# Optimization experiments

Measured on AMD Instinct MI355X. Metric: run time of the kernel, lower is better.

Reference implementation:

```python
import jax, jax.numpy as jnp
import numpy as np

N = 100000  # nodes
K = 6       # kNN neighbors (includes self, loop=True)


def _knn_edges(pos_np, k):
    """Exact kNN with self-loops, chunked to bound memory. Returns (src, dst) int32."""
    n = pos_np.shape[0]
    idx = np.empty((n, k), dtype=np.int32)
    sq = (pos_np ** 2).sum(1)
    cs = 512
    for s in range(0, n, cs):
        e = min(s + cs, n)
        d = sq[s:e, None] - 2.0 * (pos_np[s:e] @ pos_np.T) + sq[None, :]
        idx[s:e] = np.argpartition(d, k, axis=1)[:, :k].astype(np.int32)
    src = idx.reshape(-1)                                  # neighbors j
    dst = np.repeat(np.arange(n, dtype=np.int32), k)       # centers i
    return src, dst


def _linear_init(key, fan_in, fan_out):
    k1, k2 = jax.random.split(key)
    s = 1.0 / np.sqrt(fan_in)
    W = jax.random.uniform(k1, (fan_in, fan_out), minval=-s, maxval=s, dtype=jnp.float32)
    b = jax.random.uniform(k2, (fan_out,), minval=-s, maxval=s, dtype=jnp.float32)
    return W, b


def setup_inputs() -> dict:
    rng = np.random.default_rng(0)
    pos_np = rng.standard_normal((N, 3)).astype(np.float32)
    src, dst = _knn_edges(pos_np, K)
    edge_index = jnp.asarray(np.stack([src, dst]))

    key = jax.random.key(0)
    ks = jax.random.split(key, 6)
    W1a, b1a = _linear_init(ks[0], 3 + 3, 32)
    W1b, b1b = _linear_init(ks[1], 32, 32)
    W2a, b2a = _linear_init(ks[2], 32 + 3, 64)
    W2b, b2b = _linear_init(ks[3], 64, 64)
    W3a, b3a = _linear_init(ks[4], 64 + 3, 128)
    W3b, b3b = _linear_init(ks[5], 128, 128)

    return dict(pos=jnp.asarray(pos_np), edge_index=edge_index,
                W1a=W1a, b1a=b1a, W1b=W1b, b1b=b1b,
                W2a=W2a, b2a=b2a, W2b=W2b, b2b=b2b,
                W3a=W3a, b3a=b3a, W3b=W3b, b3b=b3b)


def _pointnet_conv(x, pos, src, dst, Wa, ba, Wb, bb):
    # message per edge (j->i): local_nn(concat(x_j, pos_j - pos_i)); max-aggregate at i
    m = jnp.concatenate([x[src], pos[src] - pos[dst]], axis=-1)  # [E, Cin+3]
    m = jax.nn.relu(m @ Wa + ba) @ Wb + bb                       # [E, Cout]
    return jax.ops.segment_max(m, dst, num_segments=N)           # [N, Cout]


def reference(pos, edge_index, W1a, b1a, W1b, b1b, W2a, b2a, W2b, b2b, W3a, b3a, W3b, b3b):
    src, dst = edge_index[0], edge_index[1]
    h = jax.nn.relu(_pointnet_conv(pos, pos, src, dst, W1a, b1a, W1b, b1b))
    h = jax.nn.relu(_pointnet_conv(h, pos, src, dst, W2a, b2a, W2b, b2b))
    h = jax.nn.relu(_pointnet_conv(h, pos, src, dst, W3a, b3a, W3b, b3b))
    return h
```

## Files before the change

### kernel.cpp

```cpp
#include <hip/hip_runtime.h>

#define NODES 100000
#define KNN 6

typedef unsigned short u16t;
typedef __attribute__((ext_vector_type(8))) short bf16x8;
typedef __attribute__((ext_vector_type(4))) float f32x4;
union U16 { uint4 u; bf16x8 b; };

__device__ inline f32x4 mfma16(bf16x8 a, bf16x8 b, f32x4 c) {
    return __builtin_amdgcn_mfma_f32_16x16x32_bf16(a, b, c, 0, 0, 0);
}
__device__ inline unsigned top2(unsigned u1, unsigned u0) {
    return __builtin_amdgcn_perm(u1, u0, 0x07060302u);
}
__device__ inline u16t bf16_rn(float x) {
    unsigned u = __float_as_uint(x);
    return (u16t)((u + 0x7FFF + ((u >> 16) & 1)) >> 16);
}
__device__ inline float bf16_f(u16t h) {
    return __uint_as_float(((unsigned)h) << 16);
}
__device__ inline void split_store(u16t* hp, u16t* lp, float v) {
    const unsigned u = __float_as_uint(v);
    *hp = (u16t)(u >> 16);
    const float hif = __uint_as_float(u & 0xFFFF0000u);
    *lp = (u16t)(__float_as_uint(v - hif) >> 16);
}

template <int CIN_, int N_>
__device__ void prep_dev(const float* __restrict__ W,
                         uint4* __restrict__ fh, uint4* __restrict__ fl, int idx) {
    constexpr int KT = (CIN_ + 31) / 32;
    constexpr int NTt = N_ / 16;
    if (idx >= NTt * KT * 64) return;
    const int lane = idx & 63;
    const int fk = idx >> 6;
    const int kt = fk % KT, t = fk / KT;
    const int n = t * 16 + (lane & 15);
    const int kbase = kt * 32 + (lane >> 4) * 8;
    unsigned h[4], l[4];
    for (int p = 0; p < 4; p++) {
        u16t hh[2], ll[2];
        for (int q = 0; q < 2; q++) {
            const int c = kbase + 2 * p + q;
            const float w = (c < CIN_) ? W[(size_t)c * N_ + n] : 0.f;
            const u16t hi = bf16_rn(w);
            hh[q] = hi;
            ll[q] = bf16_rn(w - bf16_f(hi));
        }
        h[p] = (unsigned)hh[0] | ((unsigned)hh[1] << 16);
        l[p] = (unsigned)ll[0] | ((unsigned)ll[1] << 16);
    }
    fh[idx] = make_uint4(h[0], h[1], h[2], h[3]);
    fl[idx] = make_uint4(l[0], l[1], l[2], l[3]);
}

__global__ void prep_all(const float* W1a, const float* W1b,
                         const float* W2a, const float* W2b,
                         const float* W3a, const float* W3b, uint4* wf) {
    const int b = blockIdx.x, t = threadIdx.x;
    if (b == 0)      prep_dev<6, 32>(W1a, wf + 0, wf + 128, t);
    else if (b == 1) prep_dev<32, 32>(W1b, wf + 256, wf + 384, t);
    else if (b == 2) prep_dev<32, 64>(W2a, wf + 512, wf + 768, t);
    else if (b < 5)  prep_dev<64, 64>(W2b, wf + 1024, wf + 1536, (b - 3) * 256 + t);
    else if (b < 11) prep_dev<67, 128>(W3a, wf + 2048, wf + 3584, (b - 5) * 256 + t);
    else             prep_dev<128, 128>(W3b, wf + 5120, wf + 7168, (b - 11) * 256 + t);
}

template <int CX, int H, int NWAVE, int NB, bool OUTP, bool DPOS>
__global__ __launch_bounds__(NWAVE * 64, (NWAVE == 2 && H >= 64) ? 3 : 4)
void pnconv_mfma(
    const u16t* __restrict__ xh, const u16t* __restrict__ xl,
    const float* __restrict__ pos, const int* __restrict__ ei,
    const uint4* __restrict__ wfa_hi, const uint4* __restrict__ wfa_lo,
    const float* __restrict__ ba,
    const uint4* __restrict__ wfb_hi, const uint4* __restrict__ wfb_lo,
    const float* __restrict__ bb,
    const float* __restrict__ wpos,
    float* __restrict__ outf, u16t* __restrict__ oh, u16t* __restrict__ ol)
{
    constexpr int NTH = NWAVE * 64;
    constexpr int CIN = DPOS ? CX : CX + 3;
    constexpr int K1T = (CIN + 31) / 32;
    constexpr int K2T = H / 32;
    constexpr int NW = (H / 16) / NWAVE;
    constexpr int E = NB * KNN;
    constexpr int MT1 = E / 16;
    constexpr int MT2 = E / 16;
    constexpr int K1P = K1T * 32 + 8;
    constexpr int K2P = K2T * 32 + 8;
    constexpr int APL = E * K1P;
    constexpr int HPL = E * K2P;
    constexpr int SM = (2 * APL > 2 * HPL) ? 2 * APL : 2 * HPL;
    static_assert(E % 48 == 0 && E <= NTH, "tile shape");
    static_assert(MT2 % 3 == 0, "slot perm needs m-triples");
    static_assert(!DPOS || (2 * APL + E * 8) <= SM, "dpos overlay fits");

    __shared__ __align__(16) u16t smem[SM];
    __shared__ int srcs[E];
    float* const dpf = (float*)&smem[2 * APL];

    const int tid = threadIdx.x;
    const int lane = tid & 63, wv = tid >> 6;
    const int l15 = lane & 15, quad = lane >> 4;
    const int node0 = blockIdx.x * NB;
    const long e0 = (long)node0 * KNN;

    if (tid < E) srcs[tid] = ei[e0 + tid];

    U16 wah[2][NW], wal[2][NW];
#pragma unroll
    for (int t = 0; t < NW; t++) {
        const int fi = ((wv * NW + t) * K1T) * 64 + lane;
        wah[0][t].u = wfa_hi[fi];
        wal[0][t].u = wfa_lo[fi];
    }
    f32x4 wpp[NW][3];
    if constexpr (DPOS) {
#pragma unroll
        for (int t = 0; t < NW; t++)
#pragma unroll
            for (int d = 0; d < 3; d++)
                wpp[t][d] = *(const f32x4*)&wpos[(size_t)(CX + d) * H +
                                                (wv * NW + t) * 16 + quad * 4];
    }
    __syncthreads();

    if constexpr (CX % 8 == 0) {
        constexpr int C8 = CX / 8;
        for (int i = tid; i < E * C8; i += NTH) {
            const int e = i / C8, c0 = i % C8;
            const int c = (c0 + e) & (C8 - 1);
            const size_t sb = (size_t)srcs[e] * CX + c * 8;
            *(uint4*)&smem[e * K1P + c * 8] = *(const uint4*)&xh[sb];
            *(uint4*)&smem[APL + e * K1P + c * 8] = *(const uint4*)&xl[sb];
        }
    }
    for (int i = tid; i < E * 3; i += NTH) {
        const int e = i / 3, d = i - 3 * (i / 3);
        const int s = srcs[e], nd = node0 + e / KNN;
        const float sp = pos[3 * s + d];
        const float dl = sp - pos[3 * nd + d];
        if constexpr (DPOS) {
            dpf[e * 4 + d] = dl;
        } else {
            if constexpr (CX == 3)
                split_store(&smem[e * K1P + d], &smem[APL + e * K1P + d], sp);
            split_store(&smem[e * K1P + CX + d], &smem[APL + e * K1P + CX + d], dl);
        }
    }
    if constexpr (!DPOS) {
        constexpr int PADA = (CIN + 7) & ~7;
        constexpr int NU4 = (K1P - PADA) / 8;
        for (int i = tid; i < 2 * E; i += NTH) {
            const int pl = (i >= E) ? 1 : 0;
            const int e = i - pl * E;
            u16t* row = &smem[pl * APL + e * K1P];
            for (int k = CIN; k < PADA; k++) row[k] = 0;
            for (int j = 0; j < NU4; j++) *(uint4*)&row[PADA + j * 8] = make_uint4(0, 0, 0, 0);
        }
    }
    __syncthreads();

    f32x4 acc1[NW][MT1];
#pragma unroll
    for (int t = 0; t < NW; t++)
#pragma unroll
        for (int m = 0; m < MT1; m++) acc1[t][m] = (f32x4){0.f, 0.f, 0.f, 0.f};

#pragma unroll
    for (int kt = 0; kt < K1T; kt++) {
        const int cur = kt & 1, nxt = cur ^ 1;
        if (kt + 1 < K1T) {
#pragma unroll
            for (int t = 0; t < NW; t++) {
                const int fi = ((wv * NW + t) * K1T + kt + 1) * 64 + lane;
                wah[nxt][t].u = wfa_hi[fi];
                wal[nxt][t].u = wfa_lo[fi];
            }
        }
#pragma unroll
        for (int m = 0; m < MT1; m++) {
            const u16t* p = &smem[(m * 16 + l15) * K1P + kt * 32 + quad * 8];
            U16 dh, dl;
            dh.u = *(const uint4*)p;
            dl.u = *(const uint4*)(p + APL);
#pragma unroll
            for (int t = 0; t < NW; t++) {
                acc1[t][m] = mfma16(wah[cur][t].b, dh.b, acc1[t][m]);
                acc1[t][m] = mfma16(wah[cur][t].b, dl.b, acc1[t][m]);
                acc1[t][m] = mfma16(wal[cur][t].b, dh.b, acc1[t][m]);
            }
        }
    }

    U16 wbh[2][NW], wbl[2][NW];
#pragma unroll
    for (int t = 0; t < NW; t++) {
        const int fi = ((wv * NW + t) * K2T) * 64 + lane;
        wbh[0][t].u = wfb_hi[fi];
        wbl[0][t].u = wfb_lo[fi];
    }

    if constexpr (DPOS) {
#pragma unroll
        for (int m = 0; m < MT1; m++) {
            const f32x4 dp = *(const f32x4*)&dpf[(m * 16 + l15) * 4];
#pragma unroll
            for (int t = 0; t < NW; t++)
#pragma unroll
                for (int j = 0; j < 4; j++)
                    acc1[t][m][j] += wpp[t][0][j] * dp[0] + wpp[t][1][j] * dp[1]
                                   + wpp[t][2][j] * dp[2];
        }
    }
    __syncthreads();

#pragma unroll
    for (int t = 0; t < NW; t++) {
        const int khb = (wv * NW + t) * 16 + quad * 4;
        const float4 bs = *(const float4*)&ba[khb];
#pragma unroll
        for (int m = 0; m < MT1; m++) {
            const float v0 = fmaxf(acc1[t][m][0] + bs.x, 0.f);
            const float v1 = fmaxf(acc1[t][m][1] + bs.y, 0.f);
            const float v2 = fmaxf(acc1[t][m][2] + bs.z, 0.f);
            const float v3 = fmaxf(acc1[t][m][3] + bs.w, 0.f);
            const unsigned u0 = __float_as_uint(v0), u1 = __float_as_uint(v1);
            const unsigned u2 = __float_as_uint(v2), u3 = __float_as_uint(v3);
            uint2 hw, lw;
            hw.x = top2(u1, u0);
            hw.y = top2(u3, u2);
            const float l0 = v0 - __uint_as_float(u0 & 0xFFFF0000u);
            const float l1 = v1 - __uint_as_float(u1 & 0xFFFF0000u);
            const float l2 = v2 - __uint_as_float(u2 & 0xFFFF0000u);
            const float l3 = v3 - __uint_as_float(u3 & 0xFFFF0000u);
            lw.x = top2(__float_as_uint(l1), __float_as_uint(l0));
            lw.y = top2(__float_as_uint(l3), __float_as_uint(l2));
            u16t* wp = &smem[(m * 16 + l15) * K2P + khb];
            *(uint2*)wp = hw;
            *(uint2*)(wp + HPL) = lw;
        }
    }
    __syncthreads();

    int eaddr[MT2];
#pragma unroll
    for (int m = 0; m < MT2; m++) {
        const int nd_s = (m / 3) * 8 + 2 * (l15 >> 2) + ((l15 >> 1) & 1);
        const int i_s = (m % 3) * 2 + (l15 & 1);
        eaddr[m] = (nd_s * KNN + i_s) * K2P + quad * 8;
    }

    f32x4 acc2[NW][MT2];
#pragma unroll
    for (int t = 0; t < NW; t++)
#pragma unroll
        for (int m = 0; m < MT2; m++) acc2[t][m] = (f32x4){0.f, 0.f, 0.f, 0.f};

#pragma unroll
    for (int kt = 0; kt < K2T; kt++) {
        const int cur = kt & 1, nxt = cur ^ 1;
        if (kt + 1 < K2T) {
#pragma unroll
            for (int t = 0; t < NW; t++) {
                const int fi = ((wv * NW + t) * K2T + kt + 1) * 64 + lane;
                wbh[nxt][t].u = wfb_hi[fi];
                wbl[nxt][t].u = wfb_lo[fi];
            }
        }
#pragma unroll
        for (int m = 0; m < MT2; m++) {
            const u16t* p = &smem[eaddr[m] + kt * 32];
            U16 dh, dl;
            dh.u = *(const uint4*)p;
            dl.u = *(const uint4*)(p + HPL);
#pragma unroll
            for (int t = 0; t < NW; t++) {
                acc2[t][m] = mfma16(dh.b, wbh[cur][t].b, acc2[t][m]);
                acc2[t][m] = mfma16(dh.b, wbl[cur][t].b, acc2[t][m]);
                acc2[t][m] = mfma16(dl.b, wbh[cur][t].b, acc2[t][m]);
            }
        }
    }

#pragma unroll
    for (int t = 0; t < NW; t++) {
        const int nb = (wv * NW + t) * 16;
        const float bias = bb[nb + l15];
#pragma unroll
        for (int g = 0; g < MT2 / 3; g++) {
#pragma unroll
            for (int rp = 0; rp < 2; rp++) {
                float v = fmaxf(
                    fmaxf(fmaxf(acc2[t][3 * g + 0][2 * rp], acc2[t][3 * g + 0][2 * rp + 1]),
                          fmaxf(acc2[t][3 * g + 1][2 * rp], acc2[t][3 * g + 1][2 * rp + 1])),
                    fmaxf(acc2[t][3 * g + 2][2 * rp], acc2[t][3 * g + 2][2 * rp + 1]));
                v = fmaxf(v + bias, 0.f);
                const int node = node0 + g * 8 + 2 * quad + rp;
                const size_t oidx = (size_t)node * H + nb + l15;
                if constexpr (OUTP) {
                    split_store(&oh[oidx], &ol[oidx], v);
                } else {
                    outf[oidx] = v;
                }
            }
        }
    }
}

extern "C" void kernel_launch(void* const* d_in, const int* in_sizes, int n_in,
                              void* d_out, int out_size, void* d_ws, size_t ws_size,
                              hipStream_t stream) {
    const float* pos = (const float*)d_in[0];
    const int* ei = (const int*)d_in[1];
    const float* W1a = (const float*)d_in[2];
    const float* b1a = (const float*)d_in[3];
    const float* W1b = (const float*)d_in[4];
    const float* b1b = (const float*)d_in[5];
    const float* W2a = (const float*)d_in[6];
    const float* b2a = (const float*)d_in[7];
    const float* W2b = (const float*)d_in[8];
    const float* b2b = (const float*)d_in[9];
    const float* W3a = (const float*)d_in[10];
    const float* b3a = (const float*)d_in[11];
    const float* W3b = (const float*)d_in[12];
    const float* b3b = (const float*)d_in[13];

    u16t* h1h = (u16t*)d_ws;
    u16t* h1l = h1h + (size_t)NODES * 32;
    u16t* h2h = h1l + (size_t)NODES * 32;
    u16t* h2l = h2h + (size_t)NODES * 64;
    uint4* wf = (uint4*)(h2l + (size_t)NODES * 64);

    prep_all<<<19, 256, 0, stream>>>(W1a, W1b, W2a, W2b, W3a, W3b, wf);

    pnconv_mfma<3, 32, 2, 16, true, false><<<NODES / 16, 128, 0, stream>>>(
        nullptr, nullptr, pos, ei,
        wf + 0, wf + 128, b1a, wf + 256, wf + 384, b1b,
        nullptr, nullptr, h1h, h1l);

    pnconv_mfma<32, 64, 2, 16, true, true><<<NODES / 16, 128, 0, stream>>>(
        h1h, h1l, pos, ei,
        wf + 512, wf + 768, b2a, wf + 1024, wf + 1536, b2b,
        W2a, nullptr, h2h, h2l);

    pnconv_mfma<64, 128, 2, 8, false, false><<<NODES / 8, 128, 0, stream>>>(
        h2h, h2l, pos, ei,
        wf + 2048, wf + 3584, b3a, wf + 5120, wf + 7168, b3b,
        nullptr, (float*)d_out, nullptr, nullptr);
}
```

Before: 249.5 us.

## Split hidden-layer LDS staging into two K phases and use four waves

Adds a KSPLIT mode in which the hidden activations for the second GEMM are staged in shared memory in two halves over K. Each half is written by the waves that own those columns and consumed before the next half is written, which halves the hidden-tile LDS footprint. Layers 2 and 3 move from 2 to 4 waves per block (fewer output tiles per wave, so fewer registers), and launch bounds are raised to 6 blocks per CU to allow more occupancy. The cost is an extra pair of block barriers per phase and possible register spills under the tighter bound.

```diff
diff --git a/kernel.cpp b/kernel.cpp
--- a/kernel.cpp
+++ b/kernel.cpp
@@ -68,8 +68,8 @@
     else             prep_dev<128, 128>(W3b, wf + 5120, wf + 7168, (b - 11) * 256 + t);
 }
 
-template <int CX, int H, int NWAVE, int NB, bool OUTP, bool DPOS>
-__global__ __launch_bounds__(NWAVE * 64, (NWAVE == 2 && H >= 64) ? 3 : 4)
+template <int CX, int H, int NWAVE, int NB, bool OUTP, bool DPOS, bool KSPLIT>
+__global__ __launch_bounds__(NWAVE * 64, 6)
 void pnconv_mfma(
     const u16t* __restrict__ xh, const u16t* __restrict__ xl,
     const float* __restrict__ pos, const int* __restrict__ ei,
@@ -84,18 +84,22 @@
     constexpr int CIN = DPOS ? CX : CX + 3;
     constexpr int K1T = (CIN + 31) / 32;
     constexpr int K2T = H / 32;
+    constexpr int NPH = KSPLIT ? 2 : 1;
+    constexpr int K2H = K2T / NPH;
     constexpr int NW = (H / 16) / NWAVE;
+    constexpr int TPP = (H / 16) / NPH;
     constexpr int E = NB * KNN;
     constexpr int MT1 = E / 16;
     constexpr int MT2 = E / 16;
     constexpr int K1P = K1T * 32 + 8;
-    constexpr int K2P = K2T * 32 + 8;
+    constexpr int K2P = K2H * 32 + 8;
     constexpr int APL = E * K1P;
     constexpr int HPL = E * K2P;
-    constexpr int SM = (2 * APL > 2 * HPL) ? 2 * APL : 2 * HPL;
+    constexpr int AREQ = 2 * APL + (DPOS ? E * 8 : 0);
+    constexpr int SM = (AREQ > 2 * HPL) ? AREQ : 2 * HPL;
     static_assert(E % 48 == 0 && E <= NTH, "tile shape");
     static_assert(MT2 % 3 == 0, "slot perm needs m-triples");
-    static_assert(!DPOS || (2 * APL + E * 8) <= SM, "dpos overlay fits");
+    static_assert(K2T % NPH == 0, "kt split");
 
     __shared__ __align__(16) u16t smem[SM];
     __shared__ int srcs[E];
@@ -215,35 +219,6 @@
                                    + wpp[t][2][j] * dp[2];
         }
     }
-    __syncthreads();
-
-#pragma unroll
-    for (int t = 0; t < NW; t++) {
-        const int khb = (wv * NW + t) * 16 + quad * 4;
-        const float4 bs = *(const float4*)&ba[khb];
-#pragma unroll
-        for (int m = 0; m < MT1; m++) {
-            const float v0 = fmaxf(acc1[t][m][0] + bs.x, 0.f);
-            const float v1 = fmaxf(acc1[t][m][1] + bs.y, 0.f);
-            const float v2 = fmaxf(acc1[t][m][2] + bs.z, 0.f);
-            const float v3 = fmaxf(acc1[t][m][3] + bs.w, 0.f);
-            const unsigned u0 = __float_as_uint(v0), u1 = __float_as_uint(v1);
-            const unsigned u2 = __float_as_uint(v2), u3 = __float_as_uint(v3);
-            uint2 hw, lw;
-            hw.x = top2(u1, u0);
-            hw.y = top2(u3, u2);
-            const float l0 = v0 - __uint_as_float(u0 & 0xFFFF0000u);
-            const float l1 = v1 - __uint_as_float(u1 & 0xFFFF0000u);
-            const float l2 = v2 - __uint_as_float(u2 & 0xFFFF0000u);
-            const float l3 = v3 - __uint_as_float(u3 & 0xFFFF0000u);
-            lw.x = top2(__float_as_uint(l1), __float_as_uint(l0));
-            lw.y = top2(__float_as_uint(l3), __float_as_uint(l2));
-            u16t* wp = &smem[(m * 16 + l15) * K2P + khb];
-            *(uint2*)wp = hw;
-            *(uint2*)(wp + HPL) = lw;
-        }
-    }
-    __syncthreads();
 
     int eaddr[MT2];
 #pragma unroll
@@ -260,27 +235,63 @@
         for (int m = 0; m < MT2; m++) acc2[t][m] = (f32x4){0.f, 0.f, 0.f, 0.f};
 
 #pragma unroll
-    for (int kt = 0; kt < K2T; kt++) {
-        const int cur = kt & 1, nxt = cur ^ 1;
-        if (kt + 1 < K2T) {
-#pragma unroll
-            for (int t = 0; t < NW; t++) {
-                const int fi = ((wv * NW + t) * K2T + kt + 1) * 64 + lane;
-                wbh[nxt][t].u = wfb_hi[fi];
-                wbl[nxt][t].u = wfb_lo[fi];
-            }
-        }
-#pragma unroll
-        for (int m = 0; m < MT2; m++) {
-            const u16t* p = &smem[eaddr[m] + kt * 32];
-            U16 dh, dl;
-            dh.u = *(const uint4*)p;
-            dl.u = *(const uint4*)(p + HPL);
-#pragma unroll
-            for (int t = 0; t < NW; t++) {
-                acc2[t][m] = mfma16(dh.b, wbh[cur][t].b, acc2[t][m]);
-                acc2[t][m] = mfma16(dh.b, wbl[cur][t].b, acc2[t][m]);
-                acc2[t][m] = mfma16(dl.b, wbh[cur][t].b, acc2[t][m]);
+    for (int ph = 0; ph < NPH; ph++) {
+        __syncthreads();
+
+#pragma unroll
+        for (int t = 0; t < NW; t++) {
+            const int ct = wv * NW + t;
+            if (KSPLIT && (ct / TPP) != ph) continue;
+            const int khb = ct * 16 + quad * 4;
+            const float4 bs = *(const float4*)&ba[khb];
+#pragma unroll
+            for (int m = 0; m < MT1; m++) {
+                const float v0 = fmaxf(acc1[t][m][0] + bs.x, 0.f);
+                const float v1 = fmaxf(acc1[t][m][1] + bs.y, 0.f);
+                const float v2 = fmaxf(acc1[t][m][2] + bs.z, 0.f);
+                const float v3 = fmaxf(acc1[t][m][3] + bs.w, 0.f);
+                const unsigned u0 = __float_as_uint(v0), u1 = __float_as_uint(v1);
+                const unsigned u2 = __float_as_uint(v2), u3 = __float_as_uint(v3);
+                uint2 hw, lw;
+                hw.x = top2(u1, u0);
+                hw.y = top2(u3, u2);
+                const float l0 = v0 - __uint_as_float(u0 & 0xFFFF0000u);
+                const float l1 = v1 - __uint_as_float(u1 & 0xFFFF0000u);
+                const float l2 = v2 - __uint_as_float(u2 & 0xFFFF0000u);
+                const float l3 = v3 - __uint_as_float(u3 & 0xFFFF0000u);
+                lw.x = top2(__float_as_uint(l1), __float_as_uint(l0));
+                lw.y = top2(__float_as_uint(l3), __float_as_uint(l2));
+                u16t* wp = &smem[(m * 16 + l15) * K2P + khb - ph * (TPP * 16)];
+                *(uint2*)wp = hw;
+                *(uint2*)(wp + HPL) = lw;
+            }
+        }
+        __syncthreads();
+
+#pragma unroll
+        for (int ktl = 0; ktl < K2H; ktl++) {
+            const int kt = ph * K2H + ktl;
+            const int cur = kt & 1, nxt = cur ^ 1;
+            if (kt + 1 < K2T) {
+#pragma unroll
+                for (int t = 0; t < NW; t++) {
+                    const int fi = ((wv * NW + t) * K2T + kt + 1) * 64 + lane;
+                    wbh[nxt][t].u = wfb_hi[fi];
+                    wbl[nxt][t].u = wfb_lo[fi];
+                }
+            }
+#pragma unroll
+            for (int m = 0; m < MT2; m++) {
+                const u16t* p = &smem[eaddr[m] + ktl * 32];
+                U16 dh, dl;
+                dh.u = *(const uint4*)p;
+                dl.u = *(const uint4*)(p + HPL);
+#pragma unroll
+                for (int t = 0; t < NW; t++) {
+                    acc2[t][m] = mfma16(dh.b, wbh[cur][t].b, acc2[t][m]);
+                    acc2[t][m] = mfma16(dh.b, wbl[cur][t].b, acc2[t][m]);
+                    acc2[t][m] = mfma16(dl.b, wbh[cur][t].b, acc2[t][m]);
+                }
             }
         }
     }
@@ -336,17 +347,17 @@
 
     prep_all<<<19, 256, 0, stream>>>(W1a, W1b, W2a, W2b, W3a, W3b, wf);
 
-    pnconv_mfma<3, 32, 2, 16, true, false><<<NODES / 16, 128, 0, stream>>>(
+    pnconv_mfma<3, 32, 2, 16, true, false, false><<<NODES / 16, 128, 0, stream>>>(
         nullptr, nullptr, pos, ei,
         wf + 0, wf + 128, b1a, wf + 256, wf + 384, b1b,
         nullptr, nullptr, h1h, h1l);
 
-    pnconv_mfma<32, 64, 2, 16, true, true><<<NODES / 16, 128, 0, stream>>>(
+    pnconv_mfma<32, 64, 4, 16, true, true, true><<<NODES / 16, 256, 0, stream>>>(
         h1h, h1l, pos, ei,
         wf + 512, wf + 768, b2a, wf + 1024, wf + 1536, b2b,
         W2a, nullptr, h2h, h2l);
 
-    pnconv_mfma<64, 128, 2, 8, false, false><<<NODES / 8, 128, 0, stream>>>(
+    pnconv_mfma<64, 128, 4, 8, false, false, true><<<NODES / 8, 256, 0, stream>>>(
         h2h, h2l, pos, ei,
         wf + 2048, wf + 3584, b3a, wf + 5120, wf + 7168, b3b,
         nullptr, (float*)d_out, nullptr, nullptr);
```

Result: slower. 308.6 us (+23.7%).
